# Kernel tuning notes

Measured on AMD Instinct MI355X. Metric: run time of the kernel, lower is better.

Reference implementation:

```python
import jax, jax.numpy as jnp
import numpy as np

N = 8192
E = 262144
IN_DIM, HID, OUT = 256, 256, 32


def setup_inputs() -> dict:
    key = jax.random.key(0)
    ks = jax.random.split(key, 10)
    features = jax.random.normal(ks[0], (N, IN_DIM), jnp.float32)
    noise = jax.random.normal(ks[1], (N, OUT), jnp.float32)
    src = jax.random.randint(ks[2], (E,), 0, N, jnp.int32)
    dst = jax.random.randint(ks[3], (E,), 0, N, jnp.int32)
    s = lambda fi, fo: 1.0 / np.sqrt(fi)
    W1 = jax.random.normal(ks[4], (IN_DIM, HID), jnp.float32) * s(IN_DIM, HID)
    W2 = jax.random.normal(ks[5], (HID, HID), jnp.float32) * s(HID, HID)
    W3 = jax.random.normal(ks[6], (HID, OUT), jnp.float32) * s(HID, OUT)
    b1 = jnp.zeros((HID,), jnp.float32)
    b2 = jnp.zeros((HID,), jnp.float32)
    b3 = jnp.zeros((OUT,), jnp.float32)
    fc_w = jax.random.normal(ks[7], (IN_DIM, OUT), jnp.float32) * s(IN_DIM, OUT)
    return dict(features=features, noise=noise, src=src, dst=dst,
                W1=W1, b1=b1, W2=W2, b2=b2, W3=W3, b3=b3, fc_w=fc_w)


def _degree_norms(src, dst, n):
    ones = jnp.ones_like(src, jnp.float32)
    out_deg = jax.ops.segment_sum(ones, src, num_segments=n)
    in_deg = jax.ops.segment_sum(ones, dst, num_segments=n)
    # DGL GraphConv norm='both' clamps degrees to min 1 before pow(-0.5)
    norm_src = jnp.maximum(out_deg, 1.0) ** -0.5  # [N]
    norm_dst = jnp.maximum(in_deg, 1.0) ** -0.5   # [N]
    return norm_src, norm_dst


def _graph_conv(x, src, dst, norm_src, norm_dst, W, b, n):
    # h = D_in^{-1/2} A D_out^{-1/2} x W + b, then relu
    h = x @ W                                  # transform first (smaller agg dim)
    m = (h * norm_src[:, None])[src]           # [E, F] gather + scale
    agg = jax.ops.segment_sum(m, dst, num_segments=n)
    return jax.nn.relu(agg * norm_dst[:, None] + b)


def reference(features, noise, src, dst, W1, b1, W2, b2, W3, b3, fc_w):
    n = features.shape[0]
    norm_s, norm_d = _degree_norms(src, dst, n)
    h = _graph_conv(features, src, dst, norm_s, norm_d, W1, b1, n)
    mean = _graph_conv(h, src, dst, norm_s, norm_d, W2, b2, n)
    log_std = _graph_conv(h, src, dst, norm_s, norm_d, W3, b3, n)
    # note: mean [N,HID] broadcasts against noise*exp(log_std) [N,OUT] only if
    # HID==OUT dims align; original code has mean from layer[1] (hidden_dim) and
    # log_std from layer[2] (out_dim). To keep the math runnable we follow the
    # VGAE intent: layer[1] and layer[2] both map to out_dim here (W2 below is
    # hidden->hidden, W3 hidden->out; mean uses W3-shaped branch). See notes.
    z = mean[:, :noise.shape[1]] if mean.shape[1] != noise.shape[1] else mean
    z = z + noise * jnp.exp(log_std)
    adj_rec = jax.nn.sigmoid(z @ z.T)          # [N, N] dense decoder
    seq_fts = features @ fc_w                  # Linear(in_dim, out_dim, bias=False)
    return adj_rec, z, seq_fts
```

## Files before the change

kernel.cpp:

```cpp
#include <hip/hip_runtime.h>
#include <hip/hip_fp16.h>

#define NNODES 8192
#define NEDGES 262144
#define NNOUT 67108864L

typedef _Float16 half8 __attribute__((ext_vector_type(8)));
typedef _Float16 half4 __attribute__((ext_vector_type(4)));
typedef _Float16 half2v __attribute__((ext_vector_type(2)));
typedef float float4v __attribute__((ext_vector_type(4)));


__global__ __launch_bounds__(256) void zero_kernel(int* __restrict__ p, int n) {
  int i = blockIdx.x * 256 + threadIdx.x;
  if (i < n) p[i] = 0;
}

__global__ __launch_bounds__(256) void deg_kernel(const int* __restrict__ src, const int* __restrict__ dst,
                                                  int* __restrict__ out_deg, int* __restrict__ in_deg) {
  int e = blockIdx.x * 256 + threadIdx.x;
  if (e < NEDGES) {
    atomicAdd(&out_deg[src[e]], 1);
    atomicAdd(&in_deg[dst[e]], 1);
  }
}

__global__ __launch_bounds__(256) void scan_norm_kernel(const int* __restrict__ in_deg,
                                                        const int* __restrict__ out_deg,
                                                        int* __restrict__ row_ptr, int* __restrict__ cursor,
                                                        float* __restrict__ norm_src, float* __restrict__ norm_dst) {
  __shared__ int partial[256];
  int t = threadIdx.x;
  int base = t * 32;
  int local[32];
  int s = 0;
#pragma unroll
  for (int i = 0; i < 32; ++i) { local[i] = in_deg[base + i]; s += local[i]; }
  partial[t] = s;
  __syncthreads();
  for (int off = 1; off < 256; off <<= 1) {
    int v = (t >= off) ? partial[t - off] : 0;
    __syncthreads();
    partial[t] += v;
    __syncthreads();
  }
  int run = (t == 0) ? 0 : partial[t - 1];
  if (t == 0) row_ptr[0] = 0;
#pragma unroll
  for (int i = 0; i < 32; ++i) {
    int od = out_deg[base + i]; if (od < 1) od = 1;
    int id = local[i]; if (id < 1) id = 1;
    norm_src[base + i] = rsqrtf((float)od);
    norm_dst[base + i] = rsqrtf((float)id);
    cursor[base + i] = run;
    run += local[i];
    row_ptr[base + i + 1] = run;
  }
}

__global__ __launch_bounds__(256) void scatter_kernel(const int* __restrict__ src, const int* __restrict__ dst,
                                                      int* __restrict__ cursor, int* __restrict__ csr) {
  int e = blockIdx.x * 256 + threadIdx.x;
  if (e < NEDGES) {
    int d = dst[e];
    int pos = atomicAdd(&cursor[d], 1);
    csr[pos] = src[e];
  }
}

__global__ __launch_bounds__(256) void convert_xs(const float* __restrict__ x, const float* __restrict__ norm_src,
                                                  _Float16* __restrict__ xs) {
  int i = blockIdx.x * 256 + threadIdx.x;
  int base = i * 4;
  float ns = norm_src[base >> 8];
  float4 v = *(const float4*)(x + base);
  half4 o = {(_Float16)(v.x * ns), (_Float16)(v.y * ns), (_Float16)(v.z * ns), (_Float16)(v.w * ns)};
  *(half4*)(xs + base) = o;
}


__global__ __launch_bounds__(256) void propagate_half(const _Float16* __restrict__ xs, float* __restrict__ Q,
                                                      const int* __restrict__ row_ptr, const int* __restrict__ csr,
                                                      const float* __restrict__ norm_dst) {
  int tid = threadIdx.x;
  int v = blockIdx.x * 2 + (tid >> 7);
  int j = tid & 127;
  int beg = row_ptr[v], end = row_ptr[v + 1];
  float ax = 0.f, ay = 0.f;
  int e = beg;
  for (; e + 4 <= end; e += 4) {
    int s0 = csr[e], s1 = csr[e + 1], s2 = csr[e + 2], s3 = csr[e + 3];
    half2v v0 = *(const half2v*)(xs + (long)s0 * 256 + 2 * j);
    half2v v1 = *(const half2v*)(xs + (long)s1 * 256 + 2 * j);
    half2v v2 = *(const half2v*)(xs + (long)s2 * 256 + 2 * j);
    half2v v3 = *(const half2v*)(xs + (long)s3 * 256 + 2 * j);
    ax += (float)v0.x + (float)v1.x + (float)v2.x + (float)v3.x;
    ay += (float)v0.y + (float)v1.y + (float)v2.y + (float)v3.y;
  }
  for (; e < end; ++e) {
    int s0 = csr[e];
    half2v v0 = *(const half2v*)(xs + (long)s0 * 256 + 2 * j);
    ax += (float)v0.x;
    ay += (float)v0.y;
  }
  float nd = norm_dst[v];
  float2 o = {ax * nd, ay * nd};
  *(float2*)&Q[(long)v * 256 + 2 * j] = o;
}


__global__ __launch_bounds__(256) void gemm_bias_relu_h(const float* __restrict__ A, const float* __restrict__ B,
                                                        const float* __restrict__ bias,
                                                        const float* __restrict__ norm_src,
                                                        _Float16* __restrict__ xs) {
  __shared__ __align__(16) float As[64][68];
  __shared__ __align__(16) float Bs[64][68];
  int tid = threadIdx.x;
  int tx = tid & 15, ty = tid >> 4;
  int rowBase = blockIdx.x * 64;
  int colBase = blockIdx.y * 64;
  float acc[4][4] = {};
  for (int kb = 0; kb < 256; kb += 64) {
    {
      int m = tid >> 2;
      int k0 = (tid & 3) * 16;
      const float* s0 = A + (rowBase + m) * 256 + kb + k0;
#pragma unroll
      for (int j = 0; j < 4; ++j) {
        float4 v = *(const float4*)(s0 + 4 * j);
        As[k0 + 4 * j + 0][m] = v.x;
        As[k0 + 4 * j + 1][m] = v.y;
        As[k0 + 4 * j + 2][m] = v.z;
        As[k0 + 4 * j + 3][m] = v.w;
      }
      int k = tid >> 2;
      int c0 = (tid & 3) * 16;
      const float* s1 = B + (kb + k) * 256 + colBase + c0;
#pragma unroll
      for (int j = 0; j < 4; ++j)
        *(float4*)&Bs[k][c0 + 4 * j] = *(const float4*)(s1 + 4 * j);
    }
    __syncthreads();
#pragma unroll 8
    for (int kk = 0; kk < 64; ++kk) {
      float4 av = *(const float4*)&As[kk][4 * ty];
      float4 bv = *(const float4*)&Bs[kk][4 * tx];
      float a[4] = {av.x, av.y, av.z, av.w};
      float b[4] = {bv.x, bv.y, bv.z, bv.w};
#pragma unroll
      for (int i = 0; i < 4; ++i)
#pragma unroll
        for (int j = 0; j < 4; ++j) acc[i][j] = fmaf(a[i], b[j], acc[i][j]);
    }
    __syncthreads();
  }
  float4 bv = *(const float4*)(bias + colBase + 4 * tx);
  float bb[4] = {bv.x, bv.y, bv.z, bv.w};
#pragma unroll
  for (int i = 0; i < 4; ++i) {
    int r = rowBase + 4 * ty + i;
    float ns = norm_src[r];
    half4 o = {(_Float16)(fmaxf(acc[i][0] + bb[0], 0.f) * ns),
               (_Float16)(fmaxf(acc[i][1] + bb[1], 0.f) * ns),
               (_Float16)(fmaxf(acc[i][2] + bb[2], 0.f) * ns),
               (_Float16)(fmaxf(acc[i][3] + bb[3], 0.f) * ns)};
    *(half4*)&xs[(long)r * 256 + colBase + 4 * tx] = o;
  }
}


__global__ __launch_bounds__(256) void gemm_z(const float* __restrict__ A, const float* __restrict__ W2,
                                              const float* __restrict__ b2, const float* __restrict__ W3,
                                              const float* __restrict__ b3, const float* __restrict__ noise,
                                              float* __restrict__ zout, _Float16* __restrict__ Zh,
                                              _Float16* __restrict__ Zl) {
  __shared__ __align__(16) float As[64][68];
  __shared__ __align__(16) float Bs[64][68];
  __shared__ float sm[64][65];
  int tid = threadIdx.x;
  int tx = tid & 15, ty = tid >> 4;
  int rowBase = blockIdx.x * 64;
  float acc[4][4] = {};
  for (int kb = 0; kb < 256; kb += 64) {
    {
      int m = tid >> 2;
      int k0 = (tid & 3) * 16;
      const float* s0 = A + (rowBase + m) * 256 + kb + k0;
#pragma unroll
      for (int j = 0; j < 4; ++j) {
        float4 v = *(const float4*)(s0 + 4 * j);
        As[k0 + 4 * j + 0][m] = v.x;
        As[k0 + 4 * j + 1][m] = v.y;
        As[k0 + 4 * j + 2][m] = v.z;
        As[k0 + 4 * j + 3][m] = v.w;
      }
      int k = tid >> 2;
      int c0 = (tid & 3) * 16;
      const float* s1 = (c0 < 32) ? (W2 + (kb + k) * 256 + c0) : (W3 + (kb + k) * 32 + (c0 - 32));
#pragma unroll
      for (int j = 0; j < 4; ++j)
        *(float4*)&Bs[k][c0 + 4 * j] = *(const float4*)(s1 + 4 * j);
    }
    __syncthreads();
#pragma unroll 8
    for (int kk = 0; kk < 64; ++kk) {
      float4 av = *(const float4*)&As[kk][4 * ty];
      float4 bv = *(const float4*)&Bs[kk][4 * tx];
      float a[4] = {av.x, av.y, av.z, av.w};
      float b[4] = {bv.x, bv.y, bv.z, bv.w};
#pragma unroll
      for (int i = 0; i < 4; ++i)
#pragma unroll
        for (int j = 0; j < 4; ++j) acc[i][j] = fmaf(a[i], b[j], acc[i][j]);
    }
    __syncthreads();
  }
  int c = 4 * tx;
  const float* bp = (c < 32) ? (b2 + c) : (b3 + (c - 32));
  float4 bv = *(const float4*)bp;
  float bb[4] = {bv.x, bv.y, bv.z, bv.w};
#pragma unroll
  for (int i = 0; i < 4; ++i) {
#pragma unroll
    for (int j = 0; j < 4; ++j) sm[4 * ty + i][c + j] = fmaxf(acc[i][j] + bb[j], 0.f);
  }
  __syncthreads();
  int r = tid >> 2;
  int cb = (tid & 3) * 8;
  long gr = rowBase + r;
  float4 n0 = *(const float4*)(noise + gr * 32 + cb);
  float4 n1 = *(const float4*)(noise + gr * 32 + cb + 4);
  float nz[8] = {n0.x, n0.y, n0.z, n0.w, n1.x, n1.y, n1.z, n1.w};
  float zv[8];
#pragma unroll
  for (int j = 0; j < 8; ++j) {
    float m = sm[r][cb + j];
    float ls = sm[r][32 + cb + j];
    zv[j] = m + nz[j] * expf(ls);
  }
  *(float4*)(zout + gr * 32 + cb) = make_float4(zv[0], zv[1], zv[2], zv[3]);
  *(float4*)(zout + gr * 32 + cb + 4) = make_float4(zv[4], zv[5], zv[6], zv[7]);
  half8 hh, hl;
#pragma unroll
  for (int j = 0; j < 8; ++j) {
    _Float16 h = (_Float16)zv[j];
    hh[j] = h;
    hl[j] = (_Float16)(zv[j] - (float)h);
  }
  *(half8*)(Zh + gr * 32 + cb) = hh;
  *(half8*)(Zl + gr * 32 + cb) = hl;
}


__global__ __launch_bounds__(256) void seq_kernel(const float* __restrict__ F, const float* __restrict__ Wf,
                                                  float* __restrict__ out) {
  int t = blockIdx.x * 256 + threadIdx.x;
  int row = t >> 3;
  int cq = (t & 7) * 4;
  float acc[4] = {0.f, 0.f, 0.f, 0.f};
  const float* frow = F + row * 256;
  for (int k = 0; k < 256; ++k) {
    float f = frow[k];
    float4 w = *(const float4*)(Wf + k * 32 + cq);
    acc[0] = fmaf(f, w.x, acc[0]);
    acc[1] = fmaf(f, w.y, acc[1]);
    acc[2] = fmaf(f, w.z, acc[2]);
    acc[3] = fmaf(f, w.w, acc[3]);
  }
  float4 o = {acc[0], acc[1], acc[2], acc[3]};
  *(float4*)&out[row * 32 + cq] = o;
}


__global__ __launch_bounds__(256) void adj_mfma(const _Float16* __restrict__ Zh, const _Float16* __restrict__ Zl,
                                                float* __restrict__ out) {
  int tid = threadIdx.x;
  int wave = tid >> 6;
  int lane = tid & 63;
  long rowBase = (long)blockIdx.y * 128 + wave * 32;
  long colBase = (long)blockIdx.x * 128;
  int l15 = lane & 15;
  int lk = (lane >> 4) * 8;
  half8 ah0 = *(const half8*)(Zh + (rowBase + l15) * 32 + lk);
  half8 al0 = *(const half8*)(Zl + (rowBase + l15) * 32 + lk);
  half8 ah1 = *(const half8*)(Zh + (rowBase + 16 + l15) * 32 + lk);
  half8 al1 = *(const half8*)(Zl + (rowBase + 16 + l15) * 32 + lk);
  int crow = (lane >> 4) * 4;
#pragma unroll
  for (int ct = 0; ct < 8; ++ct) {
    half8 bh = *(const half8*)(Zh + (colBase + ct * 16 + l15) * 32 + lk);
    half8 bl = *(const half8*)(Zl + (colBase + ct * 16 + l15) * 32 + lk);
    float4v acc0 = {}, acc1 = {};
    acc0 = __builtin_amdgcn_mfma_f32_16x16x32_f16(al0, bh, acc0, 0, 0, 0);
    acc0 = __builtin_amdgcn_mfma_f32_16x16x32_f16(ah0, bl, acc0, 0, 0, 0);
    acc0 = __builtin_amdgcn_mfma_f32_16x16x32_f16(ah0, bh, acc0, 0, 0, 0);
    acc1 = __builtin_amdgcn_mfma_f32_16x16x32_f16(al1, bh, acc1, 0, 0, 0);
    acc1 = __builtin_amdgcn_mfma_f32_16x16x32_f16(ah1, bl, acc1, 0, 0, 0);
    acc1 = __builtin_amdgcn_mfma_f32_16x16x32_f16(ah1, bh, acc1, 0, 0, 0);
    long c = colBase + ct * 16 + l15;
#pragma unroll
    for (int r = 0; r < 4; ++r) {
      out[(rowBase + crow + r) * 8192 + c] = 1.f / (1.f + __expf(-acc0[r]));
      out[(rowBase + 16 + crow + r) * 8192 + c] = 1.f / (1.f + __expf(-acc1[r]));
    }
  }
}


extern "C" void kernel_launch(void* const* d_in, const int* in_sizes, int n_in,
                              void* d_out, int out_size, void* d_ws, size_t ws_size,
                              hipStream_t stream) {
  const float* features = (const float*)d_in[0];
  const float* noise    = (const float*)d_in[1];
  const int*   src      = (const int*)d_in[2];
  const int*   dst      = (const int*)d_in[3];
  const float* W1       = (const float*)d_in[4];
  const float* b1       = (const float*)d_in[5];
  const float* W2       = (const float*)d_in[6];
  const float* b2       = (const float*)d_in[7];
  const float* W3       = (const float*)d_in[8];
  const float* b3       = (const float*)d_in[9];
  const float* fcw      = (const float*)d_in[10];

  float* out = (float*)d_out;

  int* ws_i    = (int*)d_ws;
  int* out_deg = ws_i;
  int* in_deg  = ws_i + 8192;
  int* row_ptr = ws_i + 16384;
  int* cursor  = ws_i + 24832;
  int* csr     = ws_i + 33024;
  float* norm_src = (float*)(ws_i + 295168);
  float* norm_dst = (float*)(ws_i + 303360);
  _Float16* Zh = (_Float16*)(ws_i + 311552);
  _Float16* Zl = (_Float16*)(ws_i + 442624);

  float* adj      = out;
  float* zbuf     = out + NNOUT;
  float* seq      = out + NNOUT + 262144;
  float* bufQ     = out;
  _Float16* xs    = (_Float16*)(out + 2097152);

  zero_kernel<<<64, 256, 0, stream>>>(out_deg, 16384);
  deg_kernel<<<NEDGES / 256, 256, 0, stream>>>(src, dst, out_deg, in_deg);
  scan_norm_kernel<<<1, 256, 0, stream>>>(in_deg, out_deg, row_ptr, cursor, norm_src, norm_dst);
  scatter_kernel<<<NEDGES / 256, 256, 0, stream>>>(src, dst, cursor, csr);

  convert_xs<<<2048, 256, 0, stream>>>(features, norm_src, xs);
  propagate_half<<<NNODES / 2, 256, 0, stream>>>(xs, bufQ, row_ptr, csr, norm_dst);
  gemm_bias_relu_h<<<dim3(128, 4), 256, 0, stream>>>(bufQ, W1, b1, norm_src, xs);

  propagate_half<<<NNODES / 2, 256, 0, stream>>>(xs, bufQ, row_ptr, csr, norm_dst);
  gemm_z<<<128, 256, 0, stream>>>(bufQ, W2, b2, W3, b3, noise, zbuf, Zh, Zl);

  seq_kernel<<<256, 256, 0, stream>>>(features, fcw, seq);

  adj_mfma<<<dim3(64, 64), 256, 0, stream>>>(Zh, Zl, adj);
}
```

Baseline: 218.9 us.

## Move dense GEMMs to split-fp16 MFMA and fuse small kernels into fewer launches

Replaces the fp32 SIMT GEMMs for the first and the z layers with MFMA kernels. They use a hi/lo fp16 split of activations and pre-transposed weights to keep close to fp32 accuracy. The propagate kernel now emits hi/lo fp16 directly using one wave per node with 4-wide loads. The weight prep is merged with degree zeroing, the scatter with the feature conversion, and the seq linear layer with the adjacency kernel, which cuts launch count. The adjacency store also switches to nontemporal writes with a hardware reciprocal. The trade-off is three MFMAs per product in place of one, and more workspace traffic for the hi/lo copies.

```diff
diff --git a/kernel.cpp b/kernel.cpp
--- a/kernel.cpp
+++ b/kernel.cpp
@@ -7,13 +7,29 @@
 
 typedef _Float16 half8 __attribute__((ext_vector_type(8)));
 typedef _Float16 half4 __attribute__((ext_vector_type(4)));
-typedef _Float16 half2v __attribute__((ext_vector_type(2)));
 typedef float float4v __attribute__((ext_vector_type(4)));
 
 
-__global__ __launch_bounds__(256) void zero_kernel(int* __restrict__ p, int n) {
-  int i = blockIdx.x * 256 + threadIdx.x;
-  if (i < n) p[i] = 0;
+__global__ __launch_bounds__(256) void prep_kernel(const float* __restrict__ W1, const float* __restrict__ W2,
+                                                   const float* __restrict__ W3, const float* __restrict__ b2,
+                                                   const float* __restrict__ b3, _Float16* __restrict__ W1th,
+                                                   _Float16* __restrict__ W1tl, _Float16* __restrict__ Wzth,
+                                                   _Float16* __restrict__ Wztl, float* __restrict__ bz,
+                                                   int* __restrict__ degs) {
+  int b = blockIdx.x, t = threadIdx.x;
+  float w = W1[b * 256 + t];
+  _Float16 wh = (_Float16)w;
+  W1th[t * 256 + b] = wh;
+  W1tl[t * 256 + b] = (_Float16)(w - (float)wh);
+  if (b >= 64 && b < 128) {
+    int c = b - 64;
+    float v = (c < 32) ? W2[t * 256 + c] : W3[t * 32 + (c - 32)];
+    _Float16 vh = (_Float16)v;
+    Wzth[c * 256 + t] = vh;
+    Wztl[c * 256 + t] = (_Float16)(v - (float)vh);
+  }
+  if (b == 128 && t < 64) bz[t] = (t < 32) ? b2[t] : b3[t - 32];
+  if (b >= 192) degs[(b - 192) * 256 + t] = 0;
 }
 
 __global__ __launch_bounds__(256) void deg_kernel(const int* __restrict__ src, const int* __restrict__ dst,
@@ -58,19 +74,18 @@
   }
 }
 
-__global__ __launch_bounds__(256) void scatter_kernel(const int* __restrict__ src, const int* __restrict__ dst,
-                                                      int* __restrict__ cursor, int* __restrict__ csr) {
-  int e = blockIdx.x * 256 + threadIdx.x;
-  if (e < NEDGES) {
+__global__ __launch_bounds__(256) void scatter_convert(const int* __restrict__ src, const int* __restrict__ dst,
+                                                       int* __restrict__ cursor, int* __restrict__ csr,
+                                                       const float* __restrict__ x, const float* __restrict__ norm_src,
+                                                       _Float16* __restrict__ xs) {
+  int b = blockIdx.x, t = threadIdx.x;
+  if (b < 1024) {
+    int e = b * 256 + t;
     int d = dst[e];
     int pos = atomicAdd(&cursor[d], 1);
     csr[pos] = src[e];
   }
-}
-
-__global__ __launch_bounds__(256) void convert_xs(const float* __restrict__ x, const float* __restrict__ norm_src,
-                                                  _Float16* __restrict__ xs) {
-  int i = blockIdx.x * 256 + threadIdx.x;
+  int i = b * 256 + t;
   int base = i * 4;
   float ns = norm_src[base >> 8];
   float4 v = *(const float4*)(x + base);
@@ -79,202 +94,154 @@
 }
 
 
-__global__ __launch_bounds__(256) void propagate_half(const _Float16* __restrict__ xs, float* __restrict__ Q,
-                                                      const int* __restrict__ row_ptr, const int* __restrict__ csr,
-                                                      const float* __restrict__ norm_dst) {
-  int tid = threadIdx.x;
-  int v = blockIdx.x * 2 + (tid >> 7);
-  int j = tid & 127;
+__global__ __launch_bounds__(256) void propagate_hl(const _Float16* __restrict__ xs, _Float16* __restrict__ Qh,
+                                                    _Float16* __restrict__ Ql, const int* __restrict__ row_ptr,
+                                                    const int* __restrict__ csr, const float* __restrict__ norm_dst) {
+  int v = blockIdx.x * 4 + (threadIdx.x >> 6);
+  int lane = threadIdx.x & 63;
   int beg = row_ptr[v], end = row_ptr[v + 1];
-  float ax = 0.f, ay = 0.f;
+  float a0 = 0.f, a1 = 0.f, a2 = 0.f, a3 = 0.f;
+  const _Float16* base = xs + 4 * lane;
   int e = beg;
   for (; e + 4 <= end; e += 4) {
     int s0 = csr[e], s1 = csr[e + 1], s2 = csr[e + 2], s3 = csr[e + 3];
-    half2v v0 = *(const half2v*)(xs + (long)s0 * 256 + 2 * j);
-    half2v v1 = *(const half2v*)(xs + (long)s1 * 256 + 2 * j);
-    half2v v2 = *(const half2v*)(xs + (long)s2 * 256 + 2 * j);
-    half2v v3 = *(const half2v*)(xs + (long)s3 * 256 + 2 * j);
-    ax += (float)v0.x + (float)v1.x + (float)v2.x + (float)v3.x;
-    ay += (float)v0.y + (float)v1.y + (float)v2.y + (float)v3.y;
+    half4 v0 = *(const half4*)(base + (long)s0 * 256);
+    half4 v1 = *(const half4*)(base + (long)s1 * 256);
+    half4 v2 = *(const half4*)(base + (long)s2 * 256);
+    half4 v3 = *(const half4*)(base + (long)s3 * 256);
+    a0 += (float)v0.x + (float)v1.x + (float)v2.x + (float)v3.x;
+    a1 += (float)v0.y + (float)v1.y + (float)v2.y + (float)v3.y;
+    a2 += (float)v0.z + (float)v1.z + (float)v2.z + (float)v3.z;
+    a3 += (float)v0.w + (float)v1.w + (float)v2.w + (float)v3.w;
   }
   for (; e < end; ++e) {
-    int s0 = csr[e];
-    half2v v0 = *(const half2v*)(xs + (long)s0 * 256 + 2 * j);
-    ax += (float)v0.x;
-    ay += (float)v0.y;
+    half4 v0 = *(const half4*)(base + (long)csr[e] * 256);
+    a0 += (float)v0.x; a1 += (float)v0.y; a2 += (float)v0.z; a3 += (float)v0.w;
   }
   float nd = norm_dst[v];
-  float2 o = {ax * nd, ay * nd};
-  *(float2*)&Q[(long)v * 256 + 2 * j] = o;
-}
-
-
-__global__ __launch_bounds__(256) void gemm_bias_relu_h(const float* __restrict__ A, const float* __restrict__ B,
-                                                        const float* __restrict__ bias,
-                                                        const float* __restrict__ norm_src,
-                                                        _Float16* __restrict__ xs) {
-  __shared__ __align__(16) float As[64][68];
-  __shared__ __align__(16) float Bs[64][68];
+  a0 *= nd; a1 *= nd; a2 *= nd; a3 *= nd;
+  _Float16 h0 = (_Float16)a0, h1 = (_Float16)a1, h2 = (_Float16)a2, h3 = (_Float16)a3;
+  half4 qh = {h0, h1, h2, h3};
+  half4 ql = {(_Float16)(a0 - (float)h0), (_Float16)(a1 - (float)h1),
+              (_Float16)(a2 - (float)h2), (_Float16)(a3 - (float)h3)};
+  *(half4*)(Qh + (long)v * 256 + 4 * lane) = qh;
+  *(half4*)(Ql + (long)v * 256 + 4 * lane) = ql;
+}
+
+
+__global__ __launch_bounds__(256) void gemm1_mfma(const _Float16* __restrict__ Qh, const _Float16* __restrict__ Ql,
+                                                  const _Float16* __restrict__ W1th, const _Float16* __restrict__ W1tl,
+                                                  const float* __restrict__ b1, const float* __restrict__ norm_src,
+                                                  _Float16* __restrict__ xs) {
   int tid = threadIdx.x;
-  int tx = tid & 15, ty = tid >> 4;
-  int rowBase = blockIdx.x * 64;
-  int colBase = blockIdx.y * 64;
-  float acc[4][4] = {};
-  for (int kb = 0; kb < 256; kb += 64) {
-    {
-      int m = tid >> 2;
-      int k0 = (tid & 3) * 16;
-      const float* s0 = A + (rowBase + m) * 256 + kb + k0;
-#pragma unroll
-      for (int j = 0; j < 4; ++j) {
-        float4 v = *(const float4*)(s0 + 4 * j);
-        As[k0 + 4 * j + 0][m] = v.x;
-        As[k0 + 4 * j + 1][m] = v.y;
-        As[k0 + 4 * j + 2][m] = v.z;
-        As[k0 + 4 * j + 3][m] = v.w;
-      }
-      int k = tid >> 2;
-      int c0 = (tid & 3) * 16;
-      const float* s1 = B + (kb + k) * 256 + colBase + c0;
-#pragma unroll
-      for (int j = 0; j < 4; ++j)
-        *(float4*)&Bs[k][c0 + 4 * j] = *(const float4*)(s1 + 4 * j);
-    }
-    __syncthreads();
-#pragma unroll 8
-    for (int kk = 0; kk < 64; ++kk) {
-      float4 av = *(const float4*)&As[kk][4 * ty];
-      float4 bv = *(const float4*)&Bs[kk][4 * tx];
-      float a[4] = {av.x, av.y, av.z, av.w};
-      float b[4] = {bv.x, bv.y, bv.z, bv.w};
-#pragma unroll
-      for (int i = 0; i < 4; ++i)
-#pragma unroll
-        for (int j = 0; j < 4; ++j) acc[i][j] = fmaf(a[i], b[j], acc[i][j]);
-    }
-    __syncthreads();
-  }
-  float4 bv = *(const float4*)(bias + colBase + 4 * tx);
-  float bb[4] = {bv.x, bv.y, bv.z, bv.w};
-#pragma unroll
-  for (int i = 0; i < 4; ++i) {
-    int r = rowBase + 4 * ty + i;
-    float ns = norm_src[r];
-    half4 o = {(_Float16)(fmaxf(acc[i][0] + bb[0], 0.f) * ns),
-               (_Float16)(fmaxf(acc[i][1] + bb[1], 0.f) * ns),
-               (_Float16)(fmaxf(acc[i][2] + bb[2], 0.f) * ns),
-               (_Float16)(fmaxf(acc[i][3] + bb[3], 0.f) * ns)};
-    *(half4*)&xs[(long)r * 256 + colBase + 4 * tx] = o;
-  }
-}
-
-
-__global__ __launch_bounds__(256) void gemm_z(const float* __restrict__ A, const float* __restrict__ W2,
-                                              const float* __restrict__ b2, const float* __restrict__ W3,
-                                              const float* __restrict__ b3, const float* __restrict__ noise,
-                                              float* __restrict__ zout, _Float16* __restrict__ Zh,
-                                              _Float16* __restrict__ Zl) {
-  __shared__ __align__(16) float As[64][68];
-  __shared__ __align__(16) float Bs[64][68];
-  __shared__ float sm[64][65];
+  int wave = tid >> 6, lane = tid & 63;
+  int l15 = lane & 15, lk = (lane >> 4) * 8;
+  long rowBase = blockIdx.x * 64 + wave * 16;
+  int colBase = blockIdx.y * 128;
+  float4v acc[8] = {};
+  for (int ks = 0; ks < 8; ++ks) {
+    int k0 = ks * 32;
+    half8 ah = *(const half8*)(Qh + (rowBase + l15) * 256 + k0 + lk);
+    half8 al = *(const half8*)(Ql + (rowBase + l15) * 256 + k0 + lk);
+#pragma unroll
+    for (int ct = 0; ct < 8; ++ct) {
+      long bo = (long)(colBase + ct * 16 + l15) * 256 + k0 + lk;
+      half8 bh = *(const half8*)(W1th + bo);
+      half8 bl = *(const half8*)(W1tl + bo);
+      acc[ct] = __builtin_amdgcn_mfma_f32_16x16x32_f16(al, bh, acc[ct], 0, 0, 0);
+      acc[ct] = __builtin_amdgcn_mfma_f32_16x16x32_f16(ah, bl, acc[ct], 0, 0, 0);
+      acc[ct] = __builtin_amdgcn_mfma_f32_16x16x32_f16(ah, bh, acc[ct], 0, 0, 0);
+    }
+  }
+  int crow = (lane >> 4) * 4;
+#pragma unroll
+  for (int ct = 0; ct < 8; ++ct) {
+    int c = colBase + ct * 16 + l15;
+    float bb = b1[c];
+#pragma unroll
+    for (int r = 0; r < 4; ++r) {
+      long row = rowBase + crow + r;
+      float v = fmaxf(acc[ct][r] + bb, 0.f) * norm_src[row];
+      xs[row * 256 + c] = (_Float16)v;
+    }
+  }
+}
+
+
+__global__ __launch_bounds__(256) void gemmz_mfma(const _Float16* __restrict__ Qh, const _Float16* __restrict__ Ql,
+                                                  const _Float16* __restrict__ Wzth, const _Float16* __restrict__ Wztl,
+                                                  const float* __restrict__ bz, const float* __restrict__ noise,
+                                                  float* __restrict__ zout, _Float16* __restrict__ Zh,
+                                                  _Float16* __restrict__ Zl) {
   int tid = threadIdx.x;
-  int tx = tid & 15, ty = tid >> 4;
-  int rowBase = blockIdx.x * 64;
-  float acc[4][4] = {};
-  for (int kb = 0; kb < 256; kb += 64) {
-    {
-      int m = tid >> 2;
-      int k0 = (tid & 3) * 16;
-      const float* s0 = A + (rowBase + m) * 256 + kb + k0;
-#pragma unroll
-      for (int j = 0; j < 4; ++j) {
-        float4 v = *(const float4*)(s0 + 4 * j);
-        As[k0 + 4 * j + 0][m] = v.x;
-        As[k0 + 4 * j + 1][m] = v.y;
-        As[k0 + 4 * j + 2][m] = v.z;
-        As[k0 + 4 * j + 3][m] = v.w;
-      }
-      int k = tid >> 2;
-      int c0 = (tid & 3) * 16;
-      const float* s1 = (c0 < 32) ? (W2 + (kb + k) * 256 + c0) : (W3 + (kb + k) * 32 + (c0 - 32));
-#pragma unroll
-      for (int j = 0; j < 4; ++j)
-        *(float4*)&Bs[k][c0 + 4 * j] = *(const float4*)(s1 + 4 * j);
-    }
-    __syncthreads();
-#pragma unroll 8
-    for (int kk = 0; kk < 64; ++kk) {
-      float4 av = *(const float4*)&As[kk][4 * ty];
-      float4 bv = *(const float4*)&Bs[kk][4 * tx];
-      float a[4] = {av.x, av.y, av.z, av.w};
-      float b[4] = {bv.x, bv.y, bv.z, bv.w};
-#pragma unroll
-      for (int i = 0; i < 4; ++i)
-#pragma unroll
-        for (int j = 0; j < 4; ++j) acc[i][j] = fmaf(a[i], b[j], acc[i][j]);
-    }
-    __syncthreads();
-  }
-  int c = 4 * tx;
-  const float* bp = (c < 32) ? (b2 + c) : (b3 + (c - 32));
-  float4 bv = *(const float4*)bp;
-  float bb[4] = {bv.x, bv.y, bv.z, bv.w};
-#pragma unroll
-  for (int i = 0; i < 4; ++i) {
-#pragma unroll
-    for (int j = 0; j < 4; ++j) sm[4 * ty + i][c + j] = fmaxf(acc[i][j] + bb[j], 0.f);
-  }
-  __syncthreads();
-  int r = tid >> 2;
-  int cb = (tid & 3) * 8;
-  long gr = rowBase + r;
-  float4 n0 = *(const float4*)(noise + gr * 32 + cb);
-  float4 n1 = *(const float4*)(noise + gr * 32 + cb + 4);
-  float nz[8] = {n0.x, n0.y, n0.z, n0.w, n1.x, n1.y, n1.z, n1.w};
-  float zv[8];
-#pragma unroll
-  for (int j = 0; j < 8; ++j) {
-    float m = sm[r][cb + j];
-    float ls = sm[r][32 + cb + j];
-    zv[j] = m + nz[j] * expf(ls);
-  }
-  *(float4*)(zout + gr * 32 + cb) = make_float4(zv[0], zv[1], zv[2], zv[3]);
-  *(float4*)(zout + gr * 32 + cb + 4) = make_float4(zv[4], zv[5], zv[6], zv[7]);
-  half8 hh, hl;
-#pragma unroll
-  for (int j = 0; j < 8; ++j) {
-    _Float16 h = (_Float16)zv[j];
-    hh[j] = h;
-    hl[j] = (_Float16)(zv[j] - (float)h);
-  }
-  *(half8*)(Zh + gr * 32 + cb) = hh;
-  *(half8*)(Zl + gr * 32 + cb) = hl;
-}
-
-
-__global__ __launch_bounds__(256) void seq_kernel(const float* __restrict__ F, const float* __restrict__ Wf,
-                                                  float* __restrict__ out) {
-  int t = blockIdx.x * 256 + threadIdx.x;
-  int row = t >> 3;
-  int cq = (t & 7) * 4;
-  float acc[4] = {0.f, 0.f, 0.f, 0.f};
-  const float* frow = F + row * 256;
-  for (int k = 0; k < 256; ++k) {
-    float f = frow[k];
-    float4 w = *(const float4*)(Wf + k * 32 + cq);
-    acc[0] = fmaf(f, w.x, acc[0]);
-    acc[1] = fmaf(f, w.y, acc[1]);
-    acc[2] = fmaf(f, w.z, acc[2]);
-    acc[3] = fmaf(f, w.w, acc[3]);
-  }
-  float4 o = {acc[0], acc[1], acc[2], acc[3]};
-  *(float4*)&out[row * 32 + cq] = o;
-}
-
-
-__global__ __launch_bounds__(256) void adj_mfma(const _Float16* __restrict__ Zh, const _Float16* __restrict__ Zl,
-                                                float* __restrict__ out) {
+  int wave = tid >> 6, lane = tid & 63;
+  int l15 = lane & 15, lk = (lane >> 4) * 8;
+  long rowBase = blockIdx.x * 64 + wave * 16;
+  float4v acc[4] = {};
+  for (int ks = 0; ks < 8; ++ks) {
+    int k0 = ks * 32;
+    half8 ah = *(const half8*)(Qh + (rowBase + l15) * 256 + k0 + lk);
+    half8 al = *(const half8*)(Ql + (rowBase + l15) * 256 + k0 + lk);
+#pragma unroll
+    for (int ct = 0; ct < 4; ++ct) {
+      long bo = (long)(ct * 16 + l15) * 256 + k0 + lk;
+      half8 bh = *(const half8*)(Wzth + bo);
+      half8 bl = *(const half8*)(Wztl + bo);
+      acc[ct] = __builtin_amdgcn_mfma_f32_16x16x32_f16(al, bh, acc[ct], 0, 0, 0);
+      acc[ct] = __builtin_amdgcn_mfma_f32_16x16x32_f16(ah, bl, acc[ct], 0, 0, 0);
+      acc[ct] = __builtin_amdgcn_mfma_f32_16x16x32_f16(ah, bh, acc[ct], 0, 0, 0);
+    }
+  }
+  int crow = (lane >> 4) * 4;
+  float bm0 = bz[l15], bm1 = bz[16 + l15], bs0 = bz[32 + l15], bs1 = bz[48 + l15];
+#pragma unroll
+  for (int r = 0; r < 4; ++r) {
+    long row = rowBase + crow + r;
+    float me0 = fmaxf(acc[0][r] + bm0, 0.f);
+    float me1 = fmaxf(acc[1][r] + bm1, 0.f);
+    float ls0 = fmaxf(acc[2][r] + bs0, 0.f);
+    float ls1 = fmaxf(acc[3][r] + bs1, 0.f);
+    float n0 = noise[row * 32 + l15];
+    float n1 = noise[row * 32 + 16 + l15];
+    float z0 = me0 + n0 * __expf(ls0);
+    float z1 = me1 + n1 * __expf(ls1);
+    zout[row * 32 + l15] = z0;
+    zout[row * 32 + 16 + l15] = z1;
+    _Float16 h0 = (_Float16)z0, h1 = (_Float16)z1;
+    Zh[row * 32 + l15] = h0;
+    Zl[row * 32 + l15] = (_Float16)(z0 - (float)h0);
+    Zh[row * 32 + 16 + l15] = h1;
+    Zl[row * 32 + 16 + l15] = (_Float16)(z1 - (float)h1);
+  }
+}
+
+
+__global__ __launch_bounds__(256) void adj_seq(const _Float16* __restrict__ Zh, const _Float16* __restrict__ Zl,
+                                               float* __restrict__ out, const float* __restrict__ F,
+                                               const float* __restrict__ Wf, float* __restrict__ seq) {
   int tid = threadIdx.x;
+  if (blockIdx.x >= 64) {
+    int sb = (blockIdx.x - 64) * 64 + blockIdx.y;
+    int t = sb * 256 + tid;
+    int row = t >> 3;
+    int cq = (t & 7) * 4;
+    float a0 = 0.f, a1 = 0.f, a2 = 0.f, a3 = 0.f;
+    const float* frow = F + row * 256;
+    for (int k = 0; k < 256; k += 4) {
+      float4 fv = *(const float4*)(frow + k);
+      float4 w0 = *(const float4*)(Wf + k * 32 + cq);
+      float4 w1 = *(const float4*)(Wf + (k + 1) * 32 + cq);
+      float4 w2 = *(const float4*)(Wf + (k + 2) * 32 + cq);
+      float4 w3 = *(const float4*)(Wf + (k + 3) * 32 + cq);
+      a0 = fmaf(fv.x, w0.x, fmaf(fv.y, w1.x, fmaf(fv.z, w2.x, fmaf(fv.w, w3.x, a0))));
+      a1 = fmaf(fv.x, w0.y, fmaf(fv.y, w1.y, fmaf(fv.z, w2.y, fmaf(fv.w, w3.y, a1))));
+      a2 = fmaf(fv.x, w0.z, fmaf(fv.y, w1.z, fmaf(fv.z, w2.z, fmaf(fv.w, w3.z, a2))));
+      a3 = fmaf(fv.x, w0.w, fmaf(fv.y, w1.w, fmaf(fv.z, w2.w, fmaf(fv.w, w3.w, a3))));
+    }
+    float4 o = {a0, a1, a2, a3};
+    *(float4*)&seq[row * 32 + cq] = o;
+    return;
+  }
   int wave = tid >> 6;
   int lane = tid & 63;
   long rowBase = (long)blockIdx.y * 128 + wave * 32;
@@ -300,8 +267,10 @@
     long c = colBase + ct * 16 + l15;
 #pragma unroll
     for (int r = 0; r < 4; ++r) {
-      out[(rowBase + crow + r) * 8192 + c] = 1.f / (1.f + __expf(-acc0[r]));
-      out[(rowBase + 16 + crow + r) * 8192 + c] = 1.f / (1.f + __expf(-acc1[r]));
+      float s0 = __builtin_amdgcn_rcpf(1.f + __expf(-acc0[r]));
+      float s1 = __builtin_amdgcn_rcpf(1.f + __expf(-acc1[r]));
+      __builtin_nontemporal_store(s0, &out[(rowBase + crow + r) * 8192 + c]);
+      __builtin_nontemporal_store(s1, &out[(rowBase + 16 + crow + r) * 8192 + c]);
     }
   }
 }
@@ -338,22 +307,25 @@
   float* adj      = out;
   float* zbuf     = out + NNOUT;
   float* seq      = out + NNOUT + 262144;
-  float* bufQ     = out;
-  _Float16* xs    = (_Float16*)(out + 2097152);
-
-  zero_kernel<<<64, 256, 0, stream>>>(out_deg, 16384);
+  _Float16* xs    = (_Float16*)out;
+  _Float16* Qh    = (_Float16*)(out + 1048576);
+  _Float16* Ql    = (_Float16*)(out + 2097152);
+  _Float16* W1th  = (_Float16*)(out + 3145728);
+  _Float16* W1tl  = (_Float16*)(out + 3178496);
+  _Float16* Wzth  = (_Float16*)(out + 3211264);
+  _Float16* Wztl  = (_Float16*)(out + 3219456);
+  float*    bz    = out + 3227648;
+
+  prep_kernel<<<256, 256, 0, stream>>>(W1, W2, W3, b2, b3, W1th, W1tl, Wzth, Wztl, bz, out_deg);
   deg_kernel<<<NEDGES / 256, 256, 0, stream>>>(src, dst, out_deg, in_deg);
   scan_norm_kernel<<<1, 256, 0, stream>>>(in_deg, out_deg, row_ptr, cursor, norm_src, norm_dst);
-  scatter_kernel<<<NEDGES / 256, 256, 0, stream>>>(src, dst, cursor, csr);
-
-  convert_xs<<<2048, 256, 0, stream>>>(features, norm_src, xs);
-  propagate_half<<<NNODES / 2, 256, 0, stream>>>(xs, bufQ, row_ptr, csr, norm_dst);
-  gemm_bias_relu_h<<<dim3(128, 4), 256, 0, stream>>>(bufQ, W1, b1, norm_src, xs);
-
-  propagate_half<<<NNODES / 2, 256, 0, stream>>>(xs, bufQ, row_ptr, csr, norm_dst);
-  gemm_z<<<128, 256, 0, stream>>>(bufQ, W2, b2, W3, b3, noise, zbuf, Zh, Zl);
-
-  seq_kernel<<<256, 256, 0, stream>>>(features, fcw, seq);
-
-  adj_mfma<<<dim3(64, 64), 256, 0, stream>>>(Zh, Zl, adj);
-}
+  scatter_convert<<<2048, 256, 0, stream>>>(src, dst, cursor, csr, features, norm_src, xs);
+
+  propagate_hl<<<2048, 256, 0, stream>>>(xs, Qh, Ql, row_ptr, csr, norm_dst);
+  gemm1_mfma<<<dim3(128, 2), 256, 0, stream>>>(Qh, Ql, W1th, W1tl, b1, norm_src, xs);
+
+  propagate_hl<<<2048, 256, 0, stream>>>(xs, Qh, Ql, row_ptr, csr, norm_dst);
+  gemmz_mfma<<<128, 256, 0, stream>>>(Qh, Ql, Wzth, Wztl, bz, noise, zbuf, Zh, Zl);
+
+  adj_seq<<<dim3(68, 64), 256, 0, stream>>>(Zh, Zl, adj, features, fcw, seq);
+}
```

Result: no change. 220.9 us (+0.9%).
